# Optimization experiments

Hardware: AMD Instinct MI355X
Metric: run time of the kernel (lower is better)

The kernel has to match this reference:

```python
import jax, jax.numpy as jnp
import numpy as np

RRELU_SLOPE = (1.0 / 8.0 + 1.0 / 3.0) / 2.0  # F.rrelu eval mode
N_ENT, N_REL2, H, E, B, T = 20000, 460, 128, 400000, 1024, 8


def _lin(x, W, b):
    return x @ W.T + b  # torch nn.Linear convention


def _gru_cell(x, h, w_ih, w_hh, b_ih, b_hh):
    gi = x @ w_ih.T + b_ih
    gh = h @ w_hh.T + b_hh
    i_r, i_z, i_n = jnp.split(gi, 3, axis=1)
    h_r, h_z, h_n = jnp.split(gh, 3, axis=1)
    r = jax.nn.sigmoid(i_r + h_r)
    z = jax.nn.sigmoid(i_z + h_z)
    n = jnp.tanh(i_n + r * h_n)
    return (1.0 - z) * n + z * h


def setup_inputs() -> dict:
    key = jax.random.key(0)
    ks = jax.random.split(key, 24)
    s = 0.02
    inp = {
        'ent_emb': jax.random.normal(ks[0], (N_ENT, H), jnp.float32),
        'rel_emb': jax.random.normal(ks[1], (N_REL2, H), jnp.float32),
        'weight_neighbor': jax.random.normal(ks[2], (H, H), jnp.float32) * s,
        'loop_weight': jax.random.normal(ks[3], (H, H), jnp.float32) * s,
        'evolve_loop_weight': jax.random.normal(ks[4], (H, H), jnp.float32) * s,
        'w_ih': jax.random.normal(ks[5], (3 * H, H), jnp.float32) * s,
        'w_hh': jax.random.normal(ks[6], (3 * H, H), jnp.float32) * s,
        'b_ih': jnp.zeros((3 * H,), jnp.float32),
        'b_hh': jnp.zeros((3 * H,), jnp.float32),
        'W_map1': jax.random.normal(ks[7], (2 * H, H), jnp.float32) * s,
        'b_map1': jnp.zeros((2 * H,), jnp.float32),
        'W_map2': jax.random.normal(ks[8], (H, 2 * H), jnp.float32) * s,
        'b_map2': jnp.zeros((H,), jnp.float32),
        'W_h1': jax.random.normal(ks[9], (H, H), jnp.float32) * s,
        'b_h1': jnp.zeros((H,), jnp.float32),
        'W_h2': jax.random.normal(ks[10], (H, H), jnp.float32) * s,
        'b_h2': jnp.zeros((H,), jnp.float32),
        'W_align': jax.random.normal(ks[11], (H, H), jnp.float32) * s,
        'b_align': jnp.zeros((H,), jnp.float32),
        'W_attn': jax.random.normal(ks[12], (H, H), jnp.float32) * s,
        'b_attn': jnp.zeros((H,), jnp.float32),
    }
    u = jax.random.uniform(ks[13], (B, T * N_REL2), jnp.float32)
    mask = jax.random.uniform(ks[14], (B, T * N_REL2)) > 0.7  # sparse history
    inp['partial_embeding'] = u * mask
    inp['edge_src'] = jax.random.randint(ks[15], (E,), 0, N_ENT, jnp.int32)
    inp['edge_dst'] = jax.random.randint(ks[16], (E,), 0, N_ENT, jnp.int32)
    inp['edge_type'] = jax.random.randint(ks[17], (E,), 0, N_REL2, jnp.int32)
    sub = jax.random.randint(ks[18], (B,), 0, N_ENT, jnp.int32)
    rel = jax.random.randint(ks[19], (B,), 0, N_REL2, jnp.int32)
    obj = jax.random.randint(ks[20], (B,), 0, N_ENT, jnp.int32)
    inp['triples'] = jnp.stack([sub, rel, obj], axis=1)
    return inp


def reference(ent_emb, rel_emb, weight_neighbor, loop_weight, evolve_loop_weight,
              w_ih, w_hh, b_ih, b_hh, W_map1, b_map1, W_map2, b_map2,
              W_h1, b_h1, W_h2, b_h2, W_align, b_align, W_attn, b_attn,
              partial_embeding, edge_src, edge_dst, edge_type, triples):
    # ---- UnionRGCNLayer: gather-transform-scatter ----
    h = ent_emb
    msg = (h[edge_src] + rel_emb[edge_type]) @ weight_neighbor          # [E, H]
    agg = jax.ops.segment_sum(msg, edge_dst, num_segments=N_ENT)        # [N, H]
    deg = jax.ops.segment_sum(jnp.ones((edge_dst.shape[0],), h.dtype), edge_dst,
                              num_segments=N_ENT)
    norm = jnp.where(deg > 0, 1.0 / jnp.where(deg > 0, deg, 1.0), 0.0)[:, None]
    loop = jnp.where((deg > 0)[:, None], h @ loop_weight, h @ evolve_loop_weight)
    x = agg * norm + loop
    pre_emb = jnp.where(x >= 0, x, x * RRELU_SLOPE)                     # rrelu (eval)

    # ---- PathPredictor.forward_back ----
    mapped_rel = _lin(_lin(rel_emb, W_map1, b_map1), W_map2, b_map2)    # [2R, H]
    q_rel = mapped_rel[triples[:, 1]]                                   # [B, H]
    A = _lin(q_rel, W_attn, b_attn) @ mapped_rel.T                      # [B, 2R]
    hist = partial_embeding.reshape(B, T, N_REL2).transpose(1, 0, 2)    # [T, B, 2R]

    def step(gh, cur):
        attn = cur * A
        attn = jax.nn.softmax(jnp.where(attn == 0, -1e9, attn), axis=1)
        rel_path = attn @ mapped_rel                                    # [B, H]
        return _gru_cell(rel_path, gh, w_ih, w_hh, b_ih, b_hh), None

    gru_hidden, _ = jax.lax.scan(step, jnp.zeros((B, H), pre_emb.dtype), hist)
    predicted_hist = 0.1 * _lin(_lin(q_rel, W_h1, b_h1), W_h2, b_h2) + q_rel
    match_loss = jnp.mean((predicted_hist - gru_hidden) ** 2)

    # ---- forward_forth, distmult scoring ----
    gh2 = _gru_cell(q_rel, predicted_hist, w_ih, w_hh, b_ih, b_hh)      # [B, H]
    sub_emb = pre_emb[triples[:, 0]]
    aligned_all = _lin(pre_emb, W_align, b_align)                       # [N, H]
    score_ = (_lin(sub_emb, W_align, b_align) * gh2) @ aligned_all.T    # [B, N]
    score = jax.nn.sigmoid(score_)
    # BCE(score, one_hot(obj)) without materializing labels:
    logp = jax.nn.log_sigmoid(score_)
    log1mp = jax.nn.log_sigmoid(-score_)
    total = -jnp.sum(log1mp)
    rows = jnp.arange(B)
    total = total + jnp.sum(log1mp[rows, triples[:, 2]] - logp[rows, triples[:, 2]])
    path_loss = total / (B * N_ENT)
    return score, match_loss, path_loss
```

## Files before the change

kernel.cpp:

```cpp
#include <hip/hip_runtime.h>

typedef unsigned short u16;
typedef unsigned int u32;
typedef __attribute__((ext_vector_type(8))) short bf8v;
typedef __attribute__((ext_vector_type(4))) float f4v;

#define RRELU_SLOPE 0.22916666667f

__device__ inline float bf2f(u16 u){ unsigned int i = ((unsigned int)u) << 16; float f; __builtin_memcpy(&f, &i, 4); return f; }
__device__ inline u16 f2bf(float f){ unsigned int i; __builtin_memcpy(&i, &f, 4); unsigned int r = (i + 0x7fffu + ((i >> 16) & 1u)) >> 16; return (u16)r; }
__device__ inline float frcp(float x){ return __builtin_amdgcn_rcpf(x); }
__device__ inline float fsigm(float x){ return frcp(1.f + __expf(-x)); }
__device__ inline float ftanh(float x){ return 2.f * frcp(1.f + __expf(-2.f * x)) - 1.f; }

__global__ __launch_bounds__(256) void prep_k(
    const float* __restrict__ Wn, const float* __restrict__ Wl, const float* __restrict__ We,
    const float* __restrict__ wih, const float* __restrict__ whh,
    const float* __restrict__ m1, const float* __restrict__ m2,
    const float* __restrict__ h1, const float* __restrict__ h2,
    const float* __restrict__ attn, const float* __restrict__ alg, const float* __restrict__ rel,
    const float* __restrict__ ent, const float* __restrict__ bat, const float* __restrict__ bh1,
    const int* __restrict__ edst, int E,
    u16* __restrict__ Bcat, u16* __restrict__ wihb, u16* __restrict__ whhb,
    u16* __restrict__ m1b, u16* __restrict__ m2b, u16* __restrict__ h1b, u16* __restrict__ h2b,
    u16* __restrict__ attnb, u16* __restrict__ algb, u16* __restrict__ relb,
    u16* __restrict__ entb, float* __restrict__ bias2, int* __restrict__ hist)
{
    int id = blockIdx.x * 256 + threadIdx.x;
    if (id < 49152) {
        int n = id / 384, k = id % 384;
        float v = (k < 128) ? Wn[k*128 + n] : (k < 256 ? Wl[(k-128)*128 + n] : We[(k-256)*128 + n]);
        Bcat[id] = f2bf(v); return;
    }
    id -= 49152;
    if (id < 49152) { wihb[id] = f2bf(wih[id]); return; } id -= 49152;
    if (id < 49152) { whhb[id] = f2bf(whh[id]); return; } id -= 49152;
    if (id < 32768) { m1b[id]  = f2bf(m1[id]);  return; } id -= 32768;
    if (id < 32768) { m2b[id]  = f2bf(m2[id]);  return; } id -= 32768;
    if (id < 16384) { h1b[id]  = f2bf(h1[id]);  return; } id -= 16384;
    if (id < 16384) { h2b[id]  = f2bf(h2[id]);  return; } id -= 16384;
    if (id < 16384) { attnb[id]= f2bf(attn[id]);return; } id -= 16384;
    if (id < 16384) { algb[id] = f2bf(alg[id]); return; } id -= 16384;
    if (id < 58880) { relb[id] = f2bf(rel[id]); return; } id -= 58880;
    if (id < 2560000) { entb[id] = f2bf(ent[id]); return; } id -= 2560000;
    if (id < 256) { bias2[id] = (id < 128) ? bat[id] : bh1[id - 128]; return; } id -= 256;
    if (id < E) atomicAdd(&hist[edst[id]], 1);
}

__global__ __launch_bounds__(1024) void scan_k(
    const int* __restrict__ hist, int* __restrict__ starts, int* __restrict__ cursor)
{
    __shared__ int part[1024];
    int t = threadIdx.x;
    int base = t * 20;
    int s = 0;
    for (int j = 0; j < 20; ++j) { int idx = base + j; if (idx < 20000) s += hist[idx]; }
    part[t] = s;
    __syncthreads();
    for (int off = 1; off < 1024; off <<= 1) {
        int v = (t >= off) ? part[t - off] : 0;
        __syncthreads();
        part[t] += v;
        __syncthreads();
    }
    int run = (t > 0) ? part[t - 1] : 0;
    for (int j = 0; j < 20; ++j) {
        int idx = base + j;
        if (idx < 20000) { starts[idx] = run; cursor[idx] = run; run += hist[idx]; }
    }
    if (t == 1023) starts[20000] = run;
}

__global__ __launch_bounds__(256) void scatter_k(
    const int* __restrict__ src, const int* __restrict__ dst, const int* __restrict__ typ,
    int* __restrict__ cursor, int2* __restrict__ spack, int E)
{
    int e = blockIdx.x * 256 + threadIdx.x;
    if (e >= E) return;
    int d = dst[e];
    int p = atomicAdd(&cursor[d], 1);
    spack[p] = make_int2(src[e], typ[e]);
}

__global__ __launch_bounds__(64) void agg_acat_k(
    const int2* __restrict__ spack, const int* __restrict__ starts,
    const u32* __restrict__ hb, const u32* __restrict__ rb, u32* __restrict__ Acat32)
{
    int i = blockIdx.x;
    int lane = threadIdx.x;
    int s0 = starts[i], s1 = starts[i + 1];
    float sx = 0.f, sy = 0.f;
    int e = s0;
    for (; e + 4 <= s1; e += 4) {
        int2 st0 = spack[e], st1 = spack[e+1], st2 = spack[e+2], st3 = spack[e+3];
        u32 a0 = hb[(long)st0.x * 64 + lane]; u32 r0 = rb[(long)st0.y * 64 + lane];
        u32 a1 = hb[(long)st1.x * 64 + lane]; u32 r1 = rb[(long)st1.y * 64 + lane];
        u32 a2 = hb[(long)st2.x * 64 + lane]; u32 r2 = rb[(long)st2.y * 64 + lane];
        u32 a3 = hb[(long)st3.x * 64 + lane]; u32 r3 = rb[(long)st3.y * 64 + lane];
        sx += bf2f((u16)(a0 & 0xffff)) + bf2f((u16)(r0 & 0xffff));
        sy += bf2f((u16)(a0 >> 16))    + bf2f((u16)(r0 >> 16));
        sx += bf2f((u16)(a1 & 0xffff)) + bf2f((u16)(r1 & 0xffff));
        sy += bf2f((u16)(a1 >> 16))    + bf2f((u16)(r1 >> 16));
        sx += bf2f((u16)(a2 & 0xffff)) + bf2f((u16)(r2 & 0xffff));
        sy += bf2f((u16)(a2 >> 16))    + bf2f((u16)(r2 >> 16));
        sx += bf2f((u16)(a3 & 0xffff)) + bf2f((u16)(r3 & 0xffff));
        sy += bf2f((u16)(a3 >> 16))    + bf2f((u16)(r3 >> 16));
    }
    for (; e < s1; ++e) {
        int2 st = spack[e];
        u32 a = hb[(long)st.x * 64 + lane];
        u32 r = rb[(long)st.y * 64 + lane];
        sx += bf2f((u16)(a & 0xffff)) + bf2f((u16)(r & 0xffff));
        sy += bf2f((u16)(a >> 16))    + bf2f((u16)(r >> 16));
    }
    bool has = s1 > s0;
    float nrm = has ? frcp((float)(s1 - s0)) : 0.f;
    u32 hv = hb[(long)i * 64 + lane];
    u32 agg = (u32)f2bf(sx * nrm) | ((u32)f2bf(sy * nrm) << 16);
    long o = (long)i * 192 + lane;
    Acat32[o]       = agg;
    Acat32[o + 64]  = has ? hv : 0u;
    Acat32[o + 128] = has ? 0u : hv;
}

__global__ __launch_bounds__(256) void prealn_k(
    const u16* __restrict__ acat, const u16* __restrict__ bcat,
    const u16* __restrict__ alb, const float* __restrict__ bal,
    u16* __restrict__ preb, u16* __restrict__ alnb)
{
    __shared__ u16 pl[4][16][136];
    int tid = threadIdx.x;
    int wave = tid >> 6, lane = tid & 63;
    int ln = lane & 15, q = lane >> 4;
    int bm = blockIdx.x * 64 + wave * 16;
    int am = bm + ln; if (am > 19999) am = 19999;
    const u16* Ap = acat + (long)am * 384;
    f4v acc[8] = {};
    for (int kc = 0; kc < 384; kc += 32) {
        bf8v af = *(const bf8v*)(Ap + kc + q*8);
#pragma unroll
        for (int nt = 0; nt < 8; ++nt) {
            bf8v bv = *(const bf8v*)(bcat + (nt*16 + ln)*384 + kc + q*8);
            acc[nt] = __builtin_amdgcn_mfma_f32_16x16x32_bf16(af, bv, acc[nt], 0, 0, 0);
        }
    }
#pragma unroll
    for (int nt = 0; nt < 8; ++nt) {
        int n = nt*16 + ln;
#pragma unroll
        for (int r = 0; r < 4; ++r) {
            int m = bm + q*4 + r;
            float v = acc[nt][r];
            v = (v >= 0.f) ? v : v * RRELU_SLOPE;
            u16 hv = f2bf(v);
            pl[wave][q*4 + r][n] = hv;
            if (m < 20000) preb[(long)m*128 + n] = hv;
        }
    }
    f4v acc2[8] = {};
    for (int kc = 0; kc < 128; kc += 32) {
        bf8v af = *(const bf8v*)&pl[wave][ln][kc + q*8];
#pragma unroll
        for (int nt = 0; nt < 8; ++nt) {
            bf8v bv = *(const bf8v*)(alb + (nt*16 + ln)*128 + kc + q*8);
            acc2[nt] = __builtin_amdgcn_mfma_f32_16x16x32_bf16(af, bv, acc2[nt], 0, 0, 0);
        }
    }
#pragma unroll
    for (int nt = 0; nt < 8; ++nt) {
        int n = nt*16 + ln;
        float bv = bal[n];
#pragma unroll
        for (int r = 0; r < 4; ++r) {
            int m = bm + q*4 + r;
            if (m < 20000) alnb[(long)m*128 + n] = f2bf(acc2[nt][r] + bv);
        }
    }
}

__global__ __launch_bounds__(256) void fuse_map_k(
    const u16* __restrict__ relb, const u16* __restrict__ m1b, const float* __restrict__ bm1,
    const u16* __restrict__ m2b, const float* __restrict__ bm2,
    u16* __restrict__ mapb, u16* __restrict__ mapT)
{
    __shared__ u16 t1l[4][16][264];
    int tid = threadIdx.x;
    int wave = tid >> 6, lane = tid & 63;
    int ln = lane & 15, q = lane >> 4;
    int base = blockIdx.x * 64 + wave * 16;
    int arow = base + ln; if (arow > 459) arow = 459;
    const u16* Ap = relb + arow * 128;
    f4v acc1[16] = {};
    for (int kc = 0; kc < 128; kc += 32) {
        bf8v af = *(const bf8v*)(Ap + kc + q*8);
#pragma unroll
        for (int nt = 0; nt < 16; ++nt) {
            bf8v bv = *(const bf8v*)(m1b + (nt*16 + ln)*128 + kc + q*8);
            acc1[nt] = __builtin_amdgcn_mfma_f32_16x16x32_bf16(af, bv, acc1[nt], 0, 0, 0);
        }
    }
#pragma unroll
    for (int nt = 0; nt < 16; ++nt) {
        int n = nt*16 + ln;
        float bv = bm1[n];
#pragma unroll
        for (int r = 0; r < 4; ++r)
            t1l[wave][q*4 + r][n] = f2bf(acc1[nt][r] + bv);
    }
    f4v acc2[8] = {};
    for (int kc = 0; kc < 256; kc += 32) {
        bf8v af = *(const bf8v*)&t1l[wave][ln][kc + q*8];
#pragma unroll
        for (int nt = 0; nt < 8; ++nt) {
            bf8v bv = *(const bf8v*)(m2b + (nt*16 + ln)*256 + kc + q*8);
            acc2[nt] = __builtin_amdgcn_mfma_f32_16x16x32_bf16(af, bv, acc2[nt], 0, 0, 0);
        }
    }
#pragma unroll
    for (int nt = 0; nt < 8; ++nt) {
        int n = nt*16 + ln;
        float bv = bm2[n];
#pragma unroll
        for (int r = 0; r < 4; ++r) {
            int m = base + q*4 + r;
            if (m < 460) {
                u16 hv = f2bf(acc2[nt][r] + bv);
                mapb[m*128 + n] = hv;
                mapT[n*480 + m] = hv;
            }
        }
    }
}

__global__ __launch_bounds__(256) void fuse_qt_k(
    const u16* __restrict__ mapb, const int* __restrict__ trip,
    const u16* __restrict__ atb, const float* __restrict__ bias2,
    const u16* __restrict__ h2b, const float* __restrict__ bh2,
    u16* __restrict__ atq, float* __restrict__ pred, u16* __restrict__ X)
{
    __shared__ u16 th1l[4][16][136];
    int tid = threadIdx.x;
    int wave = tid >> 6, lane = tid & 63;
    int ln = lane & 15, q = lane >> 4;
    int base = blockIdx.x * 64 + wave * 16;
    int ar = trip[(base + ln)*3 + 1];
    const u16* Ap = mapb + ar * 128;
    int rm_[4];
#pragma unroll
    for (int r = 0; r < 4; ++r) rm_[r] = trip[(base + q*4 + r)*3 + 1];
    f4v acc1[16] = {};
    for (int kc = 0; kc < 128; kc += 32) {
        bf8v af = *(const bf8v*)(Ap + kc + q*8);
#pragma unroll
        for (int nt = 0; nt < 16; ++nt) {
            bf8v bv = *(const bf8v*)(atb + (nt*16 + ln)*128 + kc + q*8);
            acc1[nt] = __builtin_amdgcn_mfma_f32_16x16x32_bf16(af, bv, acc1[nt], 0, 0, 0);
        }
    }
#pragma unroll
    for (int nt = 0; nt < 16; ++nt) {
        int n = nt*16 + ln;
        float bv = bias2[n];
#pragma unroll
        for (int r = 0; r < 4; ++r) {
            int m = base + q*4 + r;
            float x = acc1[nt][r] + bv;
            if (nt < 8) {
                atq[m*128 + n] = f2bf(x);
                X[(long)(8192 + m)*128 + n] = mapb[rm_[r]*128 + n];
            } else th1l[wave][q*4 + r][n - 128] = f2bf(x);
        }
    }
    f4v acc2[8] = {};
    for (int kc = 0; kc < 128; kc += 32) {
        bf8v af = *(const bf8v*)&th1l[wave][ln][kc + q*8];
#pragma unroll
        for (int nt = 0; nt < 8; ++nt) {
            bf8v bv = *(const bf8v*)(h2b + (nt*16 + ln)*128 + kc + q*8);
            acc2[nt] = __builtin_amdgcn_mfma_f32_16x16x32_bf16(af, bv, acc2[nt], 0, 0, 0);
        }
    }
#pragma unroll
    for (int nt = 0; nt < 8; ++nt) {
        int n = nt*16 + ln;
        float bv = bh2[n];
#pragma unroll
        for (int r = 0; r < 4; ++r) {
            int m = base + q*4 + r;
            pred[(long)m*128 + n] = 0.1f * (acc2[nt][r] + bv) + bf2f(mapb[rm_[r]*128 + n]);
        }
    }
}

__global__ __launch_bounds__(256) void smrp_k(
    const u16* __restrict__ atq, const u16* __restrict__ mapb,
    const float* __restrict__ part, const u16* __restrict__ mapT, u16* __restrict__ X)
{
    __shared__ u16 xls[32][488];
    __shared__ float asl[4][464];
    int tid = threadIdx.x;
    int wave = tid >> 6, lane = tid & 63;
    int ln = lane & 15, q = lane >> 4;
    int b0 = blockIdx.x * 4;
    {
        const u16* Ap = atq + (long)(b0 + (ln & 3)) * 128;
        bf8v af[4];
#pragma unroll
        for (int kc = 0; kc < 4; ++kc) af[kc] = *(const bf8v*)(Ap + kc*32 + q*8);
        for (int nt = wave; nt < 29; nt += 4) {
            int brow = nt*16 + ln; if (brow > 459) brow = 459;
            f4v acc = {};
#pragma unroll
            for (int kc = 0; kc < 4; ++kc) {
                bf8v bv = *(const bf8v*)(mapb + (long)brow*128 + kc*32 + q*8);
                acc = __builtin_amdgcn_mfma_f32_16x16x32_bf16(af[kc], bv, acc, 0, 0, 0);
            }
            if (q == 0) {
                int n = nt*16 + ln;
                if (n < 460) {
#pragma unroll
                    for (int r = 0; r < 4; ++r) asl[r][n] = acc[r];
                }
            }
        }
    }
    __syncthreads();
    for (int j = 0; j < 8; ++j) {
        int rl = wave*8 + j;
        int t = rl >> 2, db = rl & 3;
        const float* crow = part + (long)(b0 + db)*3680 + t*460;
        float v[8], e[8];
        float m = -1e30f;
#pragma unroll
        for (int i = 0; i < 8; ++i) {
            int r = i*64 + lane;
            if (r < 460) {
                float x = crow[r] * asl[db][r];
                x = (x == 0.f) ? -1e9f : x;
                v[i] = x; m = fmaxf(m, x);
            } else v[i] = -1e30f;
        }
#pragma unroll
        for (int off = 32; off; off >>= 1) m = fmaxf(m, __shfl_xor(m, off));
        float sum = 0.f;
#pragma unroll
        for (int i = 0; i < 8; ++i) {
            int r = i*64 + lane;
            e[i] = 0.f;
            if (r < 460) { e[i] = __expf(v[i] - m); sum += e[i]; }
        }
#pragma unroll
        for (int off = 32; off; off >>= 1) sum += __shfl_xor(sum, off);
        float inv = frcp(sum);
#pragma unroll
        for (int i = 0; i < 8; ++i) {
            int r = i*64 + lane;
            if (r < 460)      xls[rl][r] = f2bf(e[i] * inv);
            else if (r < 488) xls[rl][r] = 0;
        }
    }
    __syncthreads();
    f4v acc[2][2] = {};
    for (int kc = 0; kc < 480; kc += 32) {
        bf8v a[2], bfr[2];
#pragma unroll
        for (int mt = 0; mt < 2; ++mt)
            a[mt] = *(const bf8v*)&xls[mt*16 + ln][kc + q*8];
#pragma unroll
        for (int nt = 0; nt < 2; ++nt)
            bfr[nt] = *(const bf8v*)(mapT + (wave*32 + nt*16 + ln)*480 + kc + q*8);
#pragma unroll
        for (int mt = 0; mt < 2; ++mt)
#pragma unroll
            for (int nt = 0; nt < 2; ++nt)
                acc[mt][nt] = __builtin_amdgcn_mfma_f32_16x16x32_bf16(a[mt], bfr[nt], acc[mt][nt], 0, 0, 0);
    }
#pragma unroll
    for (int mt = 0; mt < 2; ++mt)
#pragma unroll
    for (int nt = 0; nt < 2; ++nt) {
        int n = wave*32 + nt*16 + ln;
#pragma unroll
        for (int r = 0; r < 4; ++r) {
            int rl = mt*16 + q*4 + r;
            long m = (long)(rl >> 2)*1024 + b0 + (rl & 3);
            X[m*128 + n] = f2bf(acc[mt][nt][r]);
        }
    }
}

__global__ __launch_bounds__(256, 1) void gru_k(
    const u16* __restrict__ X, const u16* __restrict__ wihb, const float* __restrict__ bih,
    const u16* __restrict__ whhb, const float* __restrict__ bhh,
    const float* __restrict__ pred,
    const u16* __restrict__ preb, const u16* __restrict__ alb, const float* __restrict__ bal,
    const u16* __restrict__ AL, const int* __restrict__ trip,
    u16* __restrict__ V, float* __restrict__ accp)
{
    __shared__ u16  hbf[16][136];
    __shared__ float hf [4][128];
    __shared__ float ghl[4][388];
    __shared__ float gil[4][388];
    __shared__ float sll[4][132];
    __shared__ float redm[4], redo[4];
    int tid = threadIdx.x;
    int wave = tid >> 6, lane = tid & 63;
    int ln = lane & 15, q = lane >> 4;
    int bb = blockIdx.x * 4;
    for (int i = tid; i < 16*136; i += 256) hbf[i/136][i%136] = 0;
    for (int i = tid; i < 4*128; i += 256) hf[i>>7][i&127] = 0.f;
    bf8v bfrag[6][4], wfrag[6][4];
#pragma unroll
    for (int nt = 0; nt < 6; ++nt)
#pragma unroll
        for (int kc = 0; kc < 4; ++kc) {
            bfrag[nt][kc] = *(const bf8v*)(whhb + (long)(wave*96 + nt*16 + ln)*128 + kc*32 + q*8);
            wfrag[nt][kc] = *(const bf8v*)(wihb + (long)(wave*96 + nt*16 + ln)*128 + kc*32 + q*8);
        }
    {
        const u16* Pp = preb + (long)trip[(bb + (ln & 3))*3 + 0] * 128;
        f4v sacc[2] = {};
#pragma unroll
        for (int kc = 0; kc < 4; ++kc) {
            bf8v pf = *(const bf8v*)(Pp + kc*32 + q*8);
#pragma unroll
            for (int nt = 0; nt < 2; ++nt) {
                bf8v bv = *(const bf8v*)(alb + (long)(wave*32 + nt*16 + ln)*128 + kc*32 + q*8);
                sacc[nt] = __builtin_amdgcn_mfma_f32_16x16x32_bf16(pf, bv, sacc[nt], 0, 0, 0);
            }
        }
        if (q == 0) {
#pragma unroll
            for (int nt = 0; nt < 2; ++nt) {
                int n = wave*32 + nt*16 + ln;
                float bv = bal[n];
#pragma unroll
                for (int r = 0; r < 4; ++r) sll[r][n] = sacc[nt][r] + bv;
            }
        }
    }
    int k = tid & 127;
    float cr = bih[k] + bhh[k];
// ... 40 lines not shown
                }
        }
        __syncthreads();
#pragma unroll
        for (int it = 0; it < 2; ++it) {
            int m = it*2 + (tid >> 7);
            float rr = fsigm(gil[m][k] + ghl[m][k] + cr);
            float zz = fsigm(gil[m][128 + k] + ghl[m][128 + k] + cz);
            float nn = ftanh(gil[m][256 + k] + bin_ + rr * (ghl[m][256 + k] + bhn));
            float hn = (1.f - zz) * nn + zz * hf[m][k];
            if (t == 7) { float d = pv[it] - hn; msum += d*d; }
            if (t == 8) {
                u16 vb = f2bf(sll[m][k] * hn);
                V[(long)(bb + m)*128 + k] = vb;
                int obj = trip[(bb + m)*3 + 2];
                osum += bf2f(vb) * bf2f(AL[(long)obj*128 + k]);
            } else { hf[m][k] = hn; hbf[m][k] = f2bf(hn); }
        }
        __syncthreads();
    }
#pragma unroll
    for (int off = 32; off; off >>= 1) { msum += __shfl_down(msum, off); osum += __shfl_down(osum, off); }
    if (lane == 0) { redm[wave] = msum; redo[wave] = osum; }
    __syncthreads();
    if (tid == 0) {
        atomicAdd(accp + 0, redm[0] + redm[1] + redm[2] + redm[3]);
        atomicAdd(accp + 2, -(redo[0] + redo[1] + redo[2] + redo[3]));
    }
}

__global__ __launch_bounds__(512) void score_k(
    const u16* __restrict__ V, const u16* __restrict__ AL,
    float* __restrict__ out, float* __restrict__ sp_acc, int N)
{
    __shared__ float stage[8][1024];
    int tid = threadIdx.x;
    int wave = tid >> 6, lane = tid & 63;
    int ln = lane & 15, q = lane >> 4;
    int bm = blockIdx.x * 128 + (wave >> 2) * 64;
    int bn = blockIdx.y * 128 + (wave & 3) * 32;
    bool valid = bn < N;
    int br[2];
#pragma unroll
    for (int nt = 0; nt < 2; ++nt) { int n = bn + nt*16 + ln; br[nt] = (n < N) ? n : (N - 1); }
    f4v acc[4][2] = {};
    for (int kc = 0; kc < 128; kc += 32) {
        bf8v a[4], b[2];
#pragma unroll
        for (int mt = 0; mt < 4; ++mt)
            a[mt] = *(const bf8v*)(V + (long)(bm + mt*16 + ln)*128 + kc + q*8);
#pragma unroll
        for (int nt = 0; nt < 2; ++nt)
            b[nt] = *(const bf8v*)(AL + (long)br[nt]*128 + kc + q*8);
#pragma unroll
        for (int mt = 0; mt < 4; ++mt)
#pragma unroll
            for (int nt = 0; nt < 2; ++nt)
                acc[mt][nt] = __builtin_amdgcn_mfma_f32_16x16x32_bf16(a[mt], b[nt], acc[mt][nt], 0, 0, 0);
    }
    float lsum = 0.f;
    float* st = stage[wave];
#pragma unroll
    for (int half = 0; half < 2; ++half) {
#pragma unroll
        for (int mh = 0; mh < 2; ++mh) {
            int mt = half*2 + mh;
#pragma unroll
            for (int nt = 0; nt < 2; ++nt)
#pragma unroll
            for (int r = 0; r < 4; ++r) {
                float s = acc[mt][nt][r];
                float e = __expf(-fabsf(s));
                float d = 1.f + e;
                float inv = frcp(d);
                st[(mh*16 + q*4 + r)*32 + nt*16 + ln] = (s >= 0.f) ? inv : e * inv;
                lsum += fmaxf(s, 0.f) + __logf(d);
            }
        }
        if (valid) {
            int row0 = lane >> 3, c4 = (lane & 7) << 2;
#pragma unroll
            for (int i = 0; i < 4; ++i) {
                int row = i*8 + row0;
                f4v vv = *(const f4v*)&st[row*32 + c4];
                __builtin_nontemporal_store(vv, (f4v*)&out[(long)(bm + half*32 + row)*N + bn + c4]);
            }
        }
    }
    if (!valid) lsum = 0.f;
#pragma unroll
    for (int off = 32; off; off >>= 1) lsum += __shfl_xor(lsum, off);
    __shared__ float red[8];
    if (lane == 0) red[wave] = lsum;
    __syncthreads();
    if (tid == 0) {
        float tsum = 0.f;
#pragma unroll
        for (int w = 0; w < 8; ++w) tsum += red[w];
        atomicAdd(sp_acc, tsum);
    }
}

__global__ void final_k(const float* __restrict__ acc, float* __restrict__ out)
{
    out[20480000] = acc[0] / (1024.f * 128.f);
    out[20480001] = (acc[1] + acc[2]) / (1024.f * 20000.f);
}

extern "C" void kernel_launch(void* const* d_in, const int* in_sizes, int n_in,
                              void* d_out, int out_size, void* d_ws, size_t ws_size,
                              hipStream_t stream)
{
    const float* ent  = (const float*)d_in[0];
    const float* rel  = (const float*)d_in[1];
    const float* Wn   = (const float*)d_in[2];
    const float* Wl   = (const float*)d_in[3];
    const float* We   = (const float*)d_in[4];
    const float* wih  = (const float*)d_in[5];
    const float* whh  = (const float*)d_in[6];
    const float* b_ih = (const float*)d_in[7];
    const float* b_hh = (const float*)d_in[8];
    const float* Wm1  = (const float*)d_in[9];
    const float* bm1  = (const float*)d_in[10];
    const float* Wm2  = (const float*)d_in[11];
    const float* bm2  = (const float*)d_in[12];
    const float* Wh1  = (const float*)d_in[13];
    const float* bh1  = (const float*)d_in[14];
    const float* Wh2  = (const float*)d_in[15];
    const float* bh2  = (const float*)d_in[16];
    const float* Wal  = (const float*)d_in[17];
    const float* bal  = (const float*)d_in[18];
    const float* Wat  = (const float*)d_in[19];
    const float* bat  = (const float*)d_in[20];
    const float* part = (const float*)d_in[21];
    const int* esrc   = (const int*)d_in[22];
    const int* edst   = (const int*)d_in[23];
    const int* etyp   = (const int*)d_in[24];
    const int* trip   = (const int*)d_in[25];
    float* out = (float*)d_out;
    const int E = in_sizes[22];

    char* ws = (char*)d_ws;
    size_t off = 0;
    auto alloc = [&](size_t bytes) { size_t o = off; off = (off + bytes + 255) & ~(size_t)255; return o; };

    size_t o_acc   = alloc(256);
    size_t o_hist  = alloc(20000 * 4);
    size_t o_mapT  = alloc(128 * 480 * 2);
    size_t zend = off;
    size_t o_starts= alloc(20004 * 4);
    size_t o_cur   = alloc(20000 * 4);
    size_t o_spack = alloc((size_t)E * 8);
    size_t o_entb  = alloc((size_t)20000 * 128 * 2);
    size_t o_acat  = alloc((size_t)20000 * 384 * 2);
    size_t o_pre   = alloc((size_t)20000 * 128 * 2);
    size_t o_aln   = alloc((size_t)20000 * 128 * 2);
    size_t o_bcat  = alloc(128 * 384 * 2);
    size_t o_wih   = alloc(384 * 128 * 2);
    size_t o_whh   = alloc(384 * 128 * 2);
    size_t o_m1    = alloc(256 * 128 * 2);
    size_t o_m2    = alloc(128 * 256 * 2);
    size_t o_ath   = alloc(2 * 128 * 128 * 2);
    size_t o_h2    = alloc(128 * 128 * 2);
    size_t o_al    = alloc(128 * 128 * 2);
    size_t o_rel   = alloc(460 * 128 * 2);
    size_t o_map   = alloc(460 * 128 * 2);
    size_t o_atq   = alloc(1024 * 128 * 2);
    size_t o_b2    = alloc(256 * 4);
    size_t o_pred  = alloc(1024 * 128 * 4);
    size_t o_X     = alloc((size_t)9216 * 128 * 2);
    size_t o_V     = alloc(1024 * 128 * 2);

    float* accp  = (float*)(ws + o_acc);
    int* histp   = (int*)(ws + o_hist);
    u16* mapT    = (u16*)(ws + o_mapT);
    int* startsp = (int*)(ws + o_starts);
    int* curp    = (int*)(ws + o_cur);
    int2* spack  = (int2*)(ws + o_spack);
    u16* entb    = (u16*)(ws + o_entb);
    u16* acat    = (u16*)(ws + o_acat);
    u16* preb    = (u16*)(ws + o_pre);
    u16* alnb    = (u16*)(ws + o_aln);
    u16* bcat    = (u16*)(ws + o_bcat);
    u16* wihb    = (u16*)(ws + o_wih);
    u16* whhb    = (u16*)(ws + o_whh);
    u16* m1b     = (u16*)(ws + o_m1);
    u16* m2b     = (u16*)(ws + o_m2);
    u16* atb     = (u16*)(ws + o_ath);
    u16* h1b     = atb + 128 * 128;
    u16* h2b     = (u16*)(ws + o_h2);
    u16* alb     = (u16*)(ws + o_al);
    u16* relb    = (u16*)(ws + o_rel);
    u16* mapb    = (u16*)(ws + o_map);
    u16* atqb    = (u16*)(ws + o_atq);
    float* bias2 = (float*)(ws + o_b2);
    float* predf = (float*)(ws + o_pred);
    u16* Xb      = (u16*)(ws + o_X);
    u16* Vb      = (u16*)(ws + o_V);

    hipMemsetAsync(ws, 0, zend, stream);

    int ptot = 2897664 + E;
    prep_k<<<(ptot + 255) / 256, 256, 0, stream>>>(
        Wn, Wl, We, wih, whh, Wm1, Wm2, Wh1, Wh2, Wat, Wal, rel,
        ent, bat, bh1, edst, E,
        bcat, wihb, whhb, m1b, m2b, h1b, h2b, atb, alb, relb,
        entb, bias2, histp);

    scan_k<<<1, 1024, 0, stream>>>(histp, startsp, curp);
    int eb = (E + 255) / 256;
    scatter_k<<<eb, 256, 0, stream>>>(esrc, edst, etyp, curp, spack, E);
    agg_acat_k<<<20000, 64, 0, stream>>>(spack, startsp, (const u32*)entb, (const u32*)relb, (u32*)acat);

    prealn_k<<<313, 256, 0, stream>>>(acat, bcat, alb, bal, preb, alnb);

    fuse_map_k<<<8, 256, 0, stream>>>(relb, m1b, bm1, m2b, bm2, mapb, mapT);

    fuse_qt_k<<<16, 256, 0, stream>>>(mapb, trip, atb, bias2, h2b, bh2, atqb, predf, Xb);

    smrp_k<<<256, 256, 0, stream>>>(atqb, mapb, part, mapT, Xb);

    gru_k<<<256, 256, 0, stream>>>(Xb, wihb, b_ih, whhb, b_hh, predf, preb, alb, bal, alnb, trip, Vb, accp);

    score_k<<<dim3(8, 157), 512, 0, stream>>>(Vb, alnb, out, accp + 1, 20000);

    final_k<<<1, 1, 0, stream>>>(accp, out);

    (void)in_sizes; (void)n_in; (void)out_size; (void)ws_size;
}
```

Measured before the change: 425.7 us.

## Fuse aggregation with pre/align GEMMs and merge independent small kernels

New measurement: 422.6 us. No clear change (-0.7%).

```diff
diff --git a/kernel.cpp b/kernel.cpp
--- a/kernel.cpp
+++ b/kernel.cpp
@@ -71,123 +71,26 @@
     if (t == 1023) starts[20000] = run;
 }
 
-__global__ __launch_bounds__(256) void scatter_k(
+__global__ __launch_bounds__(256) void scmap_k(
     const int* __restrict__ src, const int* __restrict__ dst, const int* __restrict__ typ,
-    int* __restrict__ cursor, int2* __restrict__ spack, int E)
-{
-    int e = blockIdx.x * 256 + threadIdx.x;
-    if (e >= E) return;
-    int d = dst[e];
-    int p = atomicAdd(&cursor[d], 1);
-    spack[p] = make_int2(src[e], typ[e]);
-}
-
-__global__ __launch_bounds__(64) void agg_acat_k(
-    const int2* __restrict__ spack, const int* __restrict__ starts,
-    const u32* __restrict__ hb, const u32* __restrict__ rb, u32* __restrict__ Acat32)
-{
-    int i = blockIdx.x;
-    int lane = threadIdx.x;
-    int s0 = starts[i], s1 = starts[i + 1];
-    float sx = 0.f, sy = 0.f;
-    int e = s0;
-    for (; e + 4 <= s1; e += 4) {
-        int2 st0 = spack[e], st1 = spack[e+1], st2 = spack[e+2], st3 = spack[e+3];
-        u32 a0 = hb[(long)st0.x * 64 + lane]; u32 r0 = rb[(long)st0.y * 64 + lane];
-        u32 a1 = hb[(long)st1.x * 64 + lane]; u32 r1 = rb[(long)st1.y * 64 + lane];
-        u32 a2 = hb[(long)st2.x * 64 + lane]; u32 r2 = rb[(long)st2.y * 64 + lane];
-        u32 a3 = hb[(long)st3.x * 64 + lane]; u32 r3 = rb[(long)st3.y * 64 + lane];
-        sx += bf2f((u16)(a0 & 0xffff)) + bf2f((u16)(r0 & 0xffff));
-        sy += bf2f((u16)(a0 >> 16))    + bf2f((u16)(r0 >> 16));
-        sx += bf2f((u16)(a1 & 0xffff)) + bf2f((u16)(r1 & 0xffff));
-        sy += bf2f((u16)(a1 >> 16))    + bf2f((u16)(r1 >> 16));
-        sx += bf2f((u16)(a2 & 0xffff)) + bf2f((u16)(r2 & 0xffff));
-        sy += bf2f((u16)(a2 >> 16))    + bf2f((u16)(r2 >> 16));
-        sx += bf2f((u16)(a3 & 0xffff)) + bf2f((u16)(r3 & 0xffff));
-        sy += bf2f((u16)(a3 >> 16))    + bf2f((u16)(r3 >> 16));
-    }
-    for (; e < s1; ++e) {
-        int2 st = spack[e];
-        u32 a = hb[(long)st.x * 64 + lane];
-        u32 r = rb[(long)st.y * 64 + lane];
-        sx += bf2f((u16)(a & 0xffff)) + bf2f((u16)(r & 0xffff));
-        sy += bf2f((u16)(a >> 16))    + bf2f((u16)(r >> 16));
-    }
-    bool has = s1 > s0;
-    float nrm = has ? frcp((float)(s1 - s0)) : 0.f;
-    u32 hv = hb[(long)i * 64 + lane];
-    u32 agg = (u32)f2bf(sx * nrm) | ((u32)f2bf(sy * nrm) << 16);
-    long o = (long)i * 192 + lane;
-    Acat32[o]       = agg;
-    Acat32[o + 64]  = has ? hv : 0u;
-    Acat32[o + 128] = has ? 0u : hv;
-}
-
-__global__ __launch_bounds__(256) void prealn_k(
-    const u16* __restrict__ acat, const u16* __restrict__ bcat,
-    const u16* __restrict__ alb, const float* __restrict__ bal,
-    u16* __restrict__ preb, u16* __restrict__ alnb)
-{
-    __shared__ u16 pl[4][16][136];
-    int tid = threadIdx.x;
-    int wave = tid >> 6, lane = tid & 63;
-    int ln = lane & 15, q = lane >> 4;
-    int bm = blockIdx.x * 64 + wave * 16;
-    int am = bm + ln; if (am > 19999) am = 19999;
-    const u16* Ap = acat + (long)am * 384;
-    f4v acc[8] = {};
-    for (int kc = 0; kc < 384; kc += 32) {
-        bf8v af = *(const bf8v*)(Ap + kc + q*8);
-#pragma unroll
-        for (int nt = 0; nt < 8; ++nt) {
-            bf8v bv = *(const bf8v*)(bcat + (nt*16 + ln)*384 + kc + q*8);
-            acc[nt] = __builtin_amdgcn_mfma_f32_16x16x32_bf16(af, bv, acc[nt], 0, 0, 0);
-        }
-    }
-#pragma unroll
-    for (int nt = 0; nt < 8; ++nt) {
-        int n = nt*16 + ln;
-#pragma unroll
-        for (int r = 0; r < 4; ++r) {
-            int m = bm + q*4 + r;
-            float v = acc[nt][r];
-            v = (v >= 0.f) ? v : v * RRELU_SLOPE;
-            u16 hv = f2bf(v);
-            pl[wave][q*4 + r][n] = hv;
-            if (m < 20000) preb[(long)m*128 + n] = hv;
-        }
-    }
-    f4v acc2[8] = {};
-    for (int kc = 0; kc < 128; kc += 32) {
-        bf8v af = *(const bf8v*)&pl[wave][ln][kc + q*8];
-#pragma unroll
-        for (int nt = 0; nt < 8; ++nt) {
-            bf8v bv = *(const bf8v*)(alb + (nt*16 + ln)*128 + kc + q*8);
-            acc2[nt] = __builtin_amdgcn_mfma_f32_16x16x32_bf16(af, bv, acc2[nt], 0, 0, 0);
-        }
-    }
-#pragma unroll
-    for (int nt = 0; nt < 8; ++nt) {
-        int n = nt*16 + ln;
-        float bv = bal[n];
-#pragma unroll
-        for (int r = 0; r < 4; ++r) {
-            int m = bm + q*4 + r;
-            if (m < 20000) alnb[(long)m*128 + n] = f2bf(acc2[nt][r] + bv);
-        }
-    }
-}
-
-__global__ __launch_bounds__(256) void fuse_map_k(
+    int* __restrict__ cursor, int2* __restrict__ spack, int E, int eb,
     const u16* __restrict__ relb, const u16* __restrict__ m1b, const float* __restrict__ bm1,
     const u16* __restrict__ m2b, const float* __restrict__ bm2,
     u16* __restrict__ mapb, u16* __restrict__ mapT)
 {
     __shared__ u16 t1l[4][16][264];
     int tid = threadIdx.x;
+    if ((int)blockIdx.x < eb) {
+        int e = blockIdx.x * 256 + tid;
+        if (e >= E) return;
+        int d = dst[e];
+        int p = atomicAdd(&cursor[d], 1);
+        spack[p] = make_int2(src[e], typ[e]);
+        return;
+    }
     int wave = tid >> 6, lane = tid & 63;
     int ln = lane & 15, q = lane >> 4;
-    int base = blockIdx.x * 64 + wave * 16;
+    int base = (blockIdx.x - eb) * 64 + wave * 16;
     int arow = base + ln; if (arow > 459) arow = 459;
     const u16* Ap = relb + arow * 128;
     f4v acc1[16] = {};
@@ -232,17 +135,103 @@
     }
 }
 
-__global__ __launch_bounds__(256) void fuse_qt_k(
+__global__ __launch_bounds__(256) void aggpq_k(
+    const int2* __restrict__ spack, const int* __restrict__ starts,
+    const u32* __restrict__ hb, const u32* __restrict__ rb,
+    const u16* __restrict__ bcat, const u16* __restrict__ alb, const float* __restrict__ bal,
+    u16* __restrict__ preb, u16* __restrict__ alnb,
     const u16* __restrict__ mapb, const int* __restrict__ trip,
     const u16* __restrict__ atb, const float* __restrict__ bias2,
     const u16* __restrict__ h2b, const float* __restrict__ bh2,
     u16* __restrict__ atq, float* __restrict__ pred, u16* __restrict__ X)
 {
+    __shared__ u16 acatl[16][392];
+    __shared__ u16 prel[16][136];
     __shared__ u16 th1l[4][16][136];
     int tid = threadIdx.x;
     int wave = tid >> 6, lane = tid & 63;
     int ln = lane & 15, q = lane >> 4;
-    int base = blockIdx.x * 64 + wave * 16;
+    if (blockIdx.x < 1250) {
+        int e0 = blockIdx.x * 16;
+        for (int j = 0; j < 4; ++j) {
+            int i = e0 + wave*4 + j;
+            int s0 = starts[i], s1 = starts[i + 1];
+            float sx = 0.f, sy = 0.f;
+            int e = s0;
+            for (; e + 4 <= s1; e += 4) {
+                int2 st0 = spack[e], st1 = spack[e+1], st2 = spack[e+2], st3 = spack[e+3];
+                u32 a0 = hb[(long)st0.x * 64 + lane]; u32 r0 = rb[(long)st0.y * 64 + lane];
+                u32 a1 = hb[(long)st1.x * 64 + lane]; u32 r1 = rb[(long)st1.y * 64 + lane];
+                u32 a2 = hb[(long)st2.x * 64 + lane]; u32 r2 = rb[(long)st2.y * 64 + lane];
+                u32 a3 = hb[(long)st3.x * 64 + lane]; u32 r3 = rb[(long)st3.y * 64 + lane];
+                sx += bf2f((u16)(a0 & 0xffff)) + bf2f((u16)(r0 & 0xffff));
+                sy += bf2f((u16)(a0 >> 16))    + bf2f((u16)(r0 >> 16));
+                sx += bf2f((u16)(a1 & 0xffff)) + bf2f((u16)(r1 & 0xffff));
+                sy += bf2f((u16)(a1 >> 16))    + bf2f((u16)(r1 >> 16));
+                sx += bf2f((u16)(a2 & 0xffff)) + bf2f((u16)(r2 & 0xffff));
+                sy += bf2f((u16)(a2 >> 16))    + bf2f((u16)(r2 >> 16));
+                sx += bf2f((u16)(a3 & 0xffff)) + bf2f((u16)(r3 & 0xffff));
+                sy += bf2f((u16)(a3 >> 16))    + bf2f((u16)(r3 >> 16));
+            }
+            for (; e < s1; ++e) {
+                int2 st = spack[e];
+                u32 a = hb[(long)st.x * 64 + lane];
+                u32 r = rb[(long)st.y * 64 + lane];
+                sx += bf2f((u16)(a & 0xffff)) + bf2f((u16)(r & 0xffff));
+                sy += bf2f((u16)(a >> 16))    + bf2f((u16)(r >> 16));
+            }
+            bool has = s1 > s0;
+            float nrm = has ? frcp((float)(s1 - s0)) : 0.f;
+            u32 hv = hb[(long)i * 64 + lane];
+            u32 agg = (u32)f2bf(sx * nrm) | ((u32)f2bf(sy * nrm) << 16);
+            u32* row = (u32*)&acatl[wave*4 + j][0];
+            row[lane]       = agg;
+            row[64 + lane]  = has ? hv : 0u;
+            row[128 + lane] = has ? 0u : hv;
+        }
+        __syncthreads();
+        f4v acc[2] = {};
+        for (int kc = 0; kc < 384; kc += 32) {
+            bf8v af = *(const bf8v*)&acatl[ln][kc + q*8];
+#pragma unroll
+            for (int t = 0; t < 2; ++t) {
+                bf8v bv = *(const bf8v*)(bcat + (wave*32 + t*16 + ln)*384 + kc + q*8);
+                acc[t] = __builtin_amdgcn_mfma_f32_16x16x32_bf16(af, bv, acc[t], 0, 0, 0);
+            }
+        }
+#pragma unroll
+        for (int t = 0; t < 2; ++t) {
+            int n = wave*32 + t*16 + ln;
+#pragma unroll
+            for (int r = 0; r < 4; ++r) {
+                float v = acc[t][r];
+                v = (v >= 0.f) ? v : v * RRELU_SLOPE;
+                u16 hv2 = f2bf(v);
+                prel[q*4 + r][n] = hv2;
+                preb[(long)(e0 + q*4 + r)*128 + n] = hv2;
+            }
+        }
+        __syncthreads();
+        f4v acc2[2] = {};
+        for (int kc = 0; kc < 128; kc += 32) {
+            bf8v af = *(const bf8v*)&prel[ln][kc + q*8];
+#pragma unroll
+            for (int t = 0; t < 2; ++t) {
+                bf8v bv = *(const bf8v*)(alb + (wave*32 + t*16 + ln)*128 + kc + q*8);
+                acc2[t] = __builtin_amdgcn_mfma_f32_16x16x32_bf16(af, bv, acc2[t], 0, 0, 0);
+            }
+        }
+#pragma unroll
+        for (int t = 0; t < 2; ++t) {
+            int n = wave*32 + t*16 + ln;
+            float bv = bal[n];
+#pragma unroll
+            for (int r = 0; r < 4; ++r)
+                alnb[(long)(e0 + q*4 + r)*128 + n] = f2bf(acc2[t][r] + bv);
+        }
+        return;
+    }
+    int base = (blockIdx.x - 1250) * 64 + wave * 16;
     int ar = trip[(base + ln)*3 + 1];
     const u16* Ap = mapb + ar * 128;
     int rm_[4];
@@ -634,7 +623,6 @@
     size_t o_cur   = alloc(20000 * 4);
     size_t o_spack = alloc((size_t)E * 8);
     size_t o_entb  = alloc((size_t)20000 * 128 * 2);
-    size_t o_acat  = alloc((size_t)20000 * 384 * 2);
     size_t o_pre   = alloc((size_t)20000 * 128 * 2);
     size_t o_aln   = alloc((size_t)20000 * 128 * 2);
     size_t o_bcat  = alloc(128 * 384 * 2);
@@ -660,7 +648,6 @@
     int* curp    = (int*)(ws + o_cur);
     int2* spack  = (int2*)(ws + o_spack);
     u16* entb    = (u16*)(ws + o_entb);
-    u16* acat    = (u16*)(ws + o_acat);
     u16* preb    = (u16*)(ws + o_pre);
     u16* alnb    = (u16*)(ws + o_aln);
     u16* bcat    = (u16*)(ws + o_bcat);
@@ -690,15 +677,14 @@
         entb, bias2, histp);
 
     scan_k<<<1, 1024, 0, stream>>>(histp, startsp, curp);
+
     int eb = (E + 255) / 256;
-    scatter_k<<<eb, 256, 0, stream>>>(esrc, edst, etyp, curp, spack, E);
-    agg_acat_k<<<20000, 64, 0, stream>>>(spack, startsp, (const u32*)entb, (const u32*)relb, (u32*)acat);
-
-    prealn_k<<<313, 256, 0, stream>>>(acat, bcat, alb, bal, preb, alnb);
-
-    fuse_map_k<<<8, 256, 0, stream>>>(relb, m1b, bm1, m2b, bm2, mapb, mapT);
-
-    fuse_qt_k<<<16, 256, 0, stream>>>(mapb, trip, atb, bias2, h2b, bh2, atqb, predf, Xb);
+    scmap_k<<<eb + 8, 256, 0, stream>>>(esrc, edst, etyp, curp, spack, E, eb,
+                                        relb, m1b, bm1, m2b, bm2, mapb, mapT);
+
+    aggpq_k<<<1266, 256, 0, stream>>>(spack, startsp, (const u32*)entb, (const u32*)relb,
+                                      bcat, alb, bal, preb, alnb,
+                                      mapb, trip, atb, bias2, h2b, bh2, atqb, predf, Xb);
 
     smrp_k<<<256, 256, 0, stream>>>(atqb, mapb, part, mapT, Xb);
 
```

## Merge small independent kernels into scatter and aggregation launches via block ranges

Applied to the files above, without the earlier changes.

Result: slower. 456.9 us (+7.3%).

```diff
diff --git a/kernel.cpp b/kernel.cpp
--- a/kernel.cpp
+++ b/kernel.cpp
@@ -71,56 +71,167 @@
     if (t == 1023) starts[20000] = run;
 }
 
-__global__ __launch_bounds__(256) void scatter_k(
+__global__ __launch_bounds__(256) void scmap_k(
     const int* __restrict__ src, const int* __restrict__ dst, const int* __restrict__ typ,
-    int* __restrict__ cursor, int2* __restrict__ spack, int E)
-{
-    int e = blockIdx.x * 256 + threadIdx.x;
-    if (e >= E) return;
-    int d = dst[e];
-    int p = atomicAdd(&cursor[d], 1);
-    spack[p] = make_int2(src[e], typ[e]);
-}
-
-__global__ __launch_bounds__(64) void agg_acat_k(
+    int* __restrict__ cursor, int2* __restrict__ spack, int E, int eb,
+    const u16* __restrict__ relb, const u16* __restrict__ m1b, const float* __restrict__ bm1,
+    const u16* __restrict__ m2b, const float* __restrict__ bm2,
+    u16* __restrict__ mapb, u16* __restrict__ mapT)
+{
+    __shared__ u16 t1l[4][16][264];
+    int tid = threadIdx.x;
+    if ((int)blockIdx.x < eb) {
+        int e = blockIdx.x * 256 + tid;
+        if (e >= E) return;
+        int d = dst[e];
+        int p = atomicAdd(&cursor[d], 1);
+        spack[p] = make_int2(src[e], typ[e]);
+        return;
+    }
+    int wave = tid >> 6, lane = tid & 63;
+    int ln = lane & 15, q = lane >> 4;
+    int base = (blockIdx.x - eb) * 64 + wave * 16;
+    int arow = base + ln; if (arow > 459) arow = 459;
+    const u16* Ap = relb + arow * 128;
+    f4v acc1[16] = {};
+    for (int kc = 0; kc < 128; kc += 32) {
+        bf8v af = *(const bf8v*)(Ap + kc + q*8);
+#pragma unroll
+        for (int nt = 0; nt < 16; ++nt) {
+            bf8v bv = *(const bf8v*)(m1b + (nt*16 + ln)*128 + kc + q*8);
+            acc1[nt] = __builtin_amdgcn_mfma_f32_16x16x32_bf16(af, bv, acc1[nt], 0, 0, 0);
+        }
+    }
+#pragma unroll
+    for (int nt = 0; nt < 16; ++nt) {
+        int n = nt*16 + ln;
+        float bv = bm1[n];
+#pragma unroll
+        for (int r = 0; r < 4; ++r)
+            t1l[wave][q*4 + r][n] = f2bf(acc1[nt][r] + bv);
+    }
+    f4v acc2[8] = {};
+    for (int kc = 0; kc < 256; kc += 32) {
+        bf8v af = *(const bf8v*)&t1l[wave][ln][kc + q*8];
+#pragma unroll
+        for (int nt = 0; nt < 8; ++nt) {
+            bf8v bv = *(const bf8v*)(m2b + (nt*16 + ln)*256 + kc + q*8);
+            acc2[nt] = __builtin_amdgcn_mfma_f32_16x16x32_bf16(af, bv, acc2[nt], 0, 0, 0);
+        }
+    }
+#pragma unroll
+    for (int nt = 0; nt < 8; ++nt) {
+        int n = nt*16 + ln;
+        float bv = bm2[n];
+#pragma unroll
+        for (int r = 0; r < 4; ++r) {
+            int m = base + q*4 + r;
+            if (m < 460) {
+                u16 hv = f2bf(acc2[nt][r] + bv);
+                mapb[m*128 + n] = hv;
+                mapT[n*480 + m] = hv;
+            }
+        }
+    }
+}
+
+__global__ __launch_bounds__(256) void aggq_k(
     const int2* __restrict__ spack, const int* __restrict__ starts,
-    const u32* __restrict__ hb, const u32* __restrict__ rb, u32* __restrict__ Acat32)
-{
-    int i = blockIdx.x;
-    int lane = threadIdx.x;
-    int s0 = starts[i], s1 = starts[i + 1];
-    float sx = 0.f, sy = 0.f;
-    int e = s0;
-    for (; e + 4 <= s1; e += 4) {
-        int2 st0 = spack[e], st1 = spack[e+1], st2 = spack[e+2], st3 = spack[e+3];
-        u32 a0 = hb[(long)st0.x * 64 + lane]; u32 r0 = rb[(long)st0.y * 64 + lane];
-        u32 a1 = hb[(long)st1.x * 64 + lane]; u32 r1 = rb[(long)st1.y * 64 + lane];
-        u32 a2 = hb[(long)st2.x * 64 + lane]; u32 r2 = rb[(long)st2.y * 64 + lane];
-        u32 a3 = hb[(long)st3.x * 64 + lane]; u32 r3 = rb[(long)st3.y * 64 + lane];
-        sx += bf2f((u16)(a0 & 0xffff)) + bf2f((u16)(r0 & 0xffff));
-        sy += bf2f((u16)(a0 >> 16))    + bf2f((u16)(r0 >> 16));
-        sx += bf2f((u16)(a1 & 0xffff)) + bf2f((u16)(r1 & 0xffff));
-        sy += bf2f((u16)(a1 >> 16))    + bf2f((u16)(r1 >> 16));
-        sx += bf2f((u16)(a2 & 0xffff)) + bf2f((u16)(r2 & 0xffff));
-        sy += bf2f((u16)(a2 >> 16))    + bf2f((u16)(r2 >> 16));
-        sx += bf2f((u16)(a3 & 0xffff)) + bf2f((u16)(r3 & 0xffff));
-        sy += bf2f((u16)(a3 >> 16))    + bf2f((u16)(r3 >> 16));
-    }
-    for (; e < s1; ++e) {
-        int2 st = spack[e];
-        u32 a = hb[(long)st.x * 64 + lane];
-        u32 r = rb[(long)st.y * 64 + lane];
-        sx += bf2f((u16)(a & 0xffff)) + bf2f((u16)(r & 0xffff));
-        sy += bf2f((u16)(a >> 16))    + bf2f((u16)(r >> 16));
-    }
-    bool has = s1 > s0;
-    float nrm = has ? frcp((float)(s1 - s0)) : 0.f;
-    u32 hv = hb[(long)i * 64 + lane];
-    u32 agg = (u32)f2bf(sx * nrm) | ((u32)f2bf(sy * nrm) << 16);
-    long o = (long)i * 192 + lane;
-    Acat32[o]       = agg;
-    Acat32[o + 64]  = has ? hv : 0u;
-    Acat32[o + 128] = has ? 0u : hv;
+    const u32* __restrict__ hb, const u32* __restrict__ rb, u32* __restrict__ Acat32,
+    const u16* __restrict__ mapb, const int* __restrict__ trip,
+    const u16* __restrict__ atb, const float* __restrict__ bias2,
+    const u16* __restrict__ h2b, const float* __restrict__ bh2,
+    u16* __restrict__ atq, float* __restrict__ pred, u16* __restrict__ X)
+{
+    __shared__ u16 th1l[4][16][136];
+    int tid = threadIdx.x;
+    int wave = tid >> 6, lane = tid & 63;
+    int ln = lane & 15, q = lane >> 4;
+    if (blockIdx.x < 5000) {
+        int i = blockIdx.x * 4 + wave;
+        int s0 = starts[i], s1 = starts[i + 1];
+        float sx = 0.f, sy = 0.f;
+        int e = s0;
+        for (; e + 4 <= s1; e += 4) {
+            int2 st0 = spack[e], st1 = spack[e+1], st2 = spack[e+2], st3 = spack[e+3];
+            u32 a0 = hb[(long)st0.x * 64 + lane]; u32 r0 = rb[(long)st0.y * 64 + lane];
+            u32 a1 = hb[(long)st1.x * 64 + lane]; u32 r1 = rb[(long)st1.y * 64 + lane];
+            u32 a2 = hb[(long)st2.x * 64 + lane]; u32 r2 = rb[(long)st2.y * 64 + lane];
+            u32 a3 = hb[(long)st3.x * 64 + lane]; u32 r3 = rb[(long)st3.y * 64 + lane];
+            sx += bf2f((u16)(a0 & 0xffff)) + bf2f((u16)(r0 & 0xffff));
+            sy += bf2f((u16)(a0 >> 16))    + bf2f((u16)(r0 >> 16));
+            sx += bf2f((u16)(a1 & 0xffff)) + bf2f((u16)(r1 & 0xffff));
+            sy += bf2f((u16)(a1 >> 16))    + bf2f((u16)(r1 >> 16));
+            sx += bf2f((u16)(a2 & 0xffff)) + bf2f((u16)(r2 & 0xffff));
+            sy += bf2f((u16)(a2 >> 16))    + bf2f((u16)(r2 >> 16));
+            sx += bf2f((u16)(a3 & 0xffff)) + bf2f((u16)(r3 & 0xffff));
+            sy += bf2f((u16)(a3 >> 16))    + bf2f((u16)(r3 >> 16));
+        }
+        for (; e < s1; ++e) {
+            int2 st = spack[e];
+            u32 a = hb[(long)st.x * 64 + lane];
+            u32 r = rb[(long)st.y * 64 + lane];
+            sx += bf2f((u16)(a & 0xffff)) + bf2f((u16)(r & 0xffff));
+            sy += bf2f((u16)(a >> 16))    + bf2f((u16)(r >> 16));
+        }
+        bool has = s1 > s0;
+        float nrm = has ? frcp((float)(s1 - s0)) : 0.f;
+        u32 hv = hb[(long)i * 64 + lane];
+        u32 agg = (u32)f2bf(sx * nrm) | ((u32)f2bf(sy * nrm) << 16);
+        long o = (long)i * 192 + lane;
+        Acat32[o]       = agg;
+        Acat32[o + 64]  = has ? hv : 0u;
+        Acat32[o + 128] = has ? 0u : hv;
+        return;
+    }
+    int base = (blockIdx.x - 5000) * 64 + wave * 16;
+    int ar = trip[(base + ln)*3 + 1];
+    const u16* Ap = mapb + ar * 128;
+    int rm_[4];
+#pragma unroll
+    for (int r = 0; r < 4; ++r) rm_[r] = trip[(base + q*4 + r)*3 + 1];
+    f4v acc1[16] = {};
+    for (int kc = 0; kc < 128; kc += 32) {
+        bf8v af = *(const bf8v*)(Ap + kc + q*8);
+#pragma unroll
+        for (int nt = 0; nt < 16; ++nt) {
+            bf8v bv = *(const bf8v*)(atb + (nt*16 + ln)*128 + kc + q*8);
+            acc1[nt] = __builtin_amdgcn_mfma_f32_16x16x32_bf16(af, bv, acc1[nt], 0, 0, 0);
+        }
+    }
+#pragma unroll
+    for (int nt = 0; nt < 16; ++nt) {
+        int n = nt*16 + ln;
+        float bv = bias2[n];
+#pragma unroll
+        for (int r = 0; r < 4; ++r) {
+            int m = base + q*4 + r;
+            float x = acc1[nt][r] + bv;
+            if (nt < 8) {
+                atq[m*128 + n] = f2bf(x);
+                X[(long)(8192 + m)*128 + n] = mapb[rm_[r]*128 + n];
+            } else th1l[wave][q*4 + r][n - 128] = f2bf(x);
+        }
+    }
+    f4v acc2[8] = {};
+    for (int kc = 0; kc < 128; kc += 32) {
+        bf8v af = *(const bf8v*)&th1l[wave][ln][kc + q*8];
+#pragma unroll
+        for (int nt = 0; nt < 8; ++nt) {
+            bf8v bv = *(const bf8v*)(h2b + (nt*16 + ln)*128 + kc + q*8);
+            acc2[nt] = __builtin_amdgcn_mfma_f32_16x16x32_bf16(af, bv, acc2[nt], 0, 0, 0);
+        }
+    }
+#pragma unroll
+    for (int nt = 0; nt < 8; ++nt) {
+        int n = nt*16 + ln;
+        float bv = bh2[n];
+#pragma unroll
+        for (int r = 0; r < 4; ++r) {
+            int m = base + q*4 + r;
+            pred[(long)m*128 + n] = 0.1f * (acc2[nt][r] + bv) + bf2f(mapb[rm_[r]*128 + n]);
+        }
+    }
 }
 
 __global__ __launch_bounds__(256) void prealn_k(
@@ -174,120 +285,6 @@
         for (int r = 0; r < 4; ++r) {
             int m = bm + q*4 + r;
             if (m < 20000) alnb[(long)m*128 + n] = f2bf(acc2[nt][r] + bv);
-        }
-    }
-}
-
-__global__ __launch_bounds__(256) void fuse_map_k(
-    const u16* __restrict__ relb, const u16* __restrict__ m1b, const float* __restrict__ bm1,
-    const u16* __restrict__ m2b, const float* __restrict__ bm2,
-    u16* __restrict__ mapb, u16* __restrict__ mapT)
-{
-    __shared__ u16 t1l[4][16][264];
-    int tid = threadIdx.x;
-    int wave = tid >> 6, lane = tid & 63;
-    int ln = lane & 15, q = lane >> 4;
-    int base = blockIdx.x * 64 + wave * 16;
-    int arow = base + ln; if (arow > 459) arow = 459;
-    const u16* Ap = relb + arow * 128;
-    f4v acc1[16] = {};
-    for (int kc = 0; kc < 128; kc += 32) {
-        bf8v af = *(const bf8v*)(Ap + kc + q*8);
-#pragma unroll
-        for (int nt = 0; nt < 16; ++nt) {
-            bf8v bv = *(const bf8v*)(m1b + (nt*16 + ln)*128 + kc + q*8);
-            acc1[nt] = __builtin_amdgcn_mfma_f32_16x16x32_bf16(af, bv, acc1[nt], 0, 0, 0);
-        }
-    }
-#pragma unroll
-    for (int nt = 0; nt < 16; ++nt) {
-        int n = nt*16 + ln;
-        float bv = bm1[n];
-#pragma unroll
-        for (int r = 0; r < 4; ++r)
-            t1l[wave][q*4 + r][n] = f2bf(acc1[nt][r] + bv);
-    }
-    f4v acc2[8] = {};
-    for (int kc = 0; kc < 256; kc += 32) {
-        bf8v af = *(const bf8v*)&t1l[wave][ln][kc + q*8];
-#pragma unroll
-        for (int nt = 0; nt < 8; ++nt) {
-            bf8v bv = *(const bf8v*)(m2b + (nt*16 + ln)*256 + kc + q*8);
-            acc2[nt] = __builtin_amdgcn_mfma_f32_16x16x32_bf16(af, bv, acc2[nt], 0, 0, 0);
-        }
-    }
-#pragma unroll
-    for (int nt = 0; nt < 8; ++nt) {
-        int n = nt*16 + ln;
-        float bv = bm2[n];
-#pragma unroll
-        for (int r = 0; r < 4; ++r) {
-            int m = base + q*4 + r;
-            if (m < 460) {
-                u16 hv = f2bf(acc2[nt][r] + bv);
-                mapb[m*128 + n] = hv;
-                mapT[n*480 + m] = hv;
-            }
-        }
-    }
-}
-
-__global__ __launch_bounds__(256) void fuse_qt_k(
-    const u16* __restrict__ mapb, const int* __restrict__ trip,
-    const u16* __restrict__ atb, const float* __restrict__ bias2,
-    const u16* __restrict__ h2b, const float* __restrict__ bh2,
-    u16* __restrict__ atq, float* __restrict__ pred, u16* __restrict__ X)
-{
-    __shared__ u16 th1l[4][16][136];
-    int tid = threadIdx.x;
-    int wave = tid >> 6, lane = tid & 63;
-    int ln = lane & 15, q = lane >> 4;
-    int base = blockIdx.x * 64 + wave * 16;
-    int ar = trip[(base + ln)*3 + 1];
-    const u16* Ap = mapb + ar * 128;
-    int rm_[4];
-#pragma unroll
-    for (int r = 0; r < 4; ++r) rm_[r] = trip[(base + q*4 + r)*3 + 1];
-    f4v acc1[16] = {};
-    for (int kc = 0; kc < 128; kc += 32) {
-        bf8v af = *(const bf8v*)(Ap + kc + q*8);
-#pragma unroll
-        for (int nt = 0; nt < 16; ++nt) {
-            bf8v bv = *(const bf8v*)(atb + (nt*16 + ln)*128 + kc + q*8);
-            acc1[nt] = __builtin_amdgcn_mfma_f32_16x16x32_bf16(af, bv, acc1[nt], 0, 0, 0);
-        }
-    }
-#pragma unroll
-    for (int nt = 0; nt < 16; ++nt) {
-        int n = nt*16 + ln;
-        float bv = bias2[n];
-#pragma unroll
-        for (int r = 0; r < 4; ++r) {
-            int m = base + q*4 + r;
-            float x = acc1[nt][r] + bv;
-            if (nt < 8) {
-                atq[m*128 + n] = f2bf(x);
-                X[(long)(8192 + m)*128 + n] = mapb[rm_[r]*128 + n];
-            } else th1l[wave][q*4 + r][n - 128] = f2bf(x);
-        }
-    }
-    f4v acc2[8] = {};
-    for (int kc = 0; kc < 128; kc += 32) {
-        bf8v af = *(const bf8v*)&th1l[wave][ln][kc + q*8];
-#pragma unroll
-        for (int nt = 0; nt < 8; ++nt) {
-            bf8v bv = *(const bf8v*)(h2b + (nt*16 + ln)*128 + kc + q*8);
-            acc2[nt] = __builtin_amdgcn_mfma_f32_16x16x32_bf16(af, bv, acc2[nt], 0, 0, 0);
-        }
-    }
-#pragma unroll
-    for (int nt = 0; nt < 8; ++nt) {
-        int n = nt*16 + ln;
-        float bv = bh2[n];
-#pragma unroll
-        for (int r = 0; r < 4; ++r) {
-            int m = base + q*4 + r;
-            pred[(long)m*128 + n] = 0.1f * (acc2[nt][r] + bv) + bf2f(mapb[rm_[r]*128 + n]);
         }
     }
 }
@@ -690,16 +687,16 @@
         entb, bias2, histp);
 
     scan_k<<<1, 1024, 0, stream>>>(histp, startsp, curp);
+
     int eb = (E + 255) / 256;
-    scatter_k<<<eb, 256, 0, stream>>>(esrc, edst, etyp, curp, spack, E);
-    agg_acat_k<<<20000, 64, 0, stream>>>(spack, startsp, (const u32*)entb, (const u32*)relb, (u32*)acat);
+    scmap_k<<<eb + 8, 256, 0, stream>>>(esrc, edst, etyp, curp, spack, E, eb,
+                                        relb, m1b, bm1, m2b, bm2, mapb, mapT);
+
+    aggq_k<<<5016, 256, 0, stream>>>(spack, startsp, (const u32*)entb, (const u32*)relb, (u32*)acat,
+                                     mapb, trip, atb, bias2, h2b, bh2, atqb, predf, Xb);
 
     prealn_k<<<313, 256, 0, stream>>>(acat, bcat, alb, bal, preb, alnb);
 
-    fuse_map_k<<<8, 256, 0, stream>>>(relb, m1b, bm1, m2b, bm2, mapb, mapT);
-
-    fuse_qt_k<<<16, 256, 0, stream>>>(mapb, trip, atb, bias2, h2b, bh2, atqb, predf, Xb);
-
     smrp_k<<<256, 256, 0, stream>>>(atqb, mapb, part, mapT, Xb);
 
     gru_k<<<256, 256, 0, stream>>>(Xb, wihb, b_ih, whhb, b_hh, predf, preb, alb, bal, alnb, trip, Vb, accp);
```
